# Optimization experiments

Hardware: AMD Instinct MI355X
Metric: run time of the kernel (lower is better)

The kernel has to match this reference:

```python
import jax, jax.numpy as jnp
import numpy as np

C1 = 512  # channels1 (query input dim)
C = 512   # channels (model dim)


def setup_inputs() -> dict:
    key = jax.random.key(0)
    ks = jax.random.split(key, 12)
    B, Lq, Lk = 8, 2048, 2048
    s1 = 1.0 / np.sqrt(C1)
    s = 1.0 / np.sqrt(C)
    return {
        "rep": jax.random.normal(ks[0], (B, Lq, C1), dtype=jnp.float32),
        "rep1": jax.random.normal(ks[1], (B, Lk, C), dtype=jnp.float32),
        "Wq_w": jax.random.uniform(ks[2], (C1, C), jnp.float32, -s1, s1),
        "Wq_b": jax.random.uniform(ks[3], (C,), jnp.float32, -s1, s1),
        "Wk_w": jax.random.uniform(ks[4], (C, C), jnp.float32, -s, s),
        "Wk_b": jax.random.uniform(ks[5], (C,), jnp.float32, -s, s),
        "Wv_w": jax.random.uniform(ks[6], (C, C), jnp.float32, -s, s),
        "Wv_b": jax.random.uniform(ks[7], (C,), jnp.float32, -s, s),
        "FC_w": jax.random.uniform(ks[8], (C, C), jnp.float32, -s, s),
        "FC_b": jax.random.uniform(ks[9], (C,), jnp.float32, -s, s),
    }


def reference(rep, rep1, Wq_w, Wq_b, Wk_w, Wk_b, Wv_w, Wv_b, FC_w, FC_b):
    # Linear + ReLU projections (single head)
    q = jax.nn.relu(jnp.einsum('blc,cd->bld', rep, Wq_w) + Wq_b)    # [B,Lq,C]
    k = jax.nn.relu(jnp.einsum('blc,cd->bld', rep1, Wk_w) + Wk_b)   # [B,Lk,C]
    v = jax.nn.relu(jnp.einsum('blc,cd->bld', rep1, Wv_w) + Wv_b)   # [B,Lk,C]
    scores = jnp.einsum('bqd,bkd->bqk', q, k) / jnp.sqrt(jnp.float32(C))
    attn = jax.nn.softmax(scores, axis=-1)                           # [B,Lq,Lk]
    out = jnp.einsum('bqk,bkd->bqd', attn, v)                        # [B,Lq,C]
    out = jax.nn.relu(jnp.einsum('bld,de->ble', out, FC_w) + FC_b)
    return out
```

## Files before the change

### kernel.cpp

```cpp
#include <hip/hip_runtime.h>


typedef __attribute__((ext_vector_type(8))) short short8;
typedef __attribute__((ext_vector_type(4))) float f32x4;

#define SEQ 2048
#define CH 512
#define NB 8
#define MTOT (NB * SEQ)

#define GLDS16(gp, lp)                                                                  \
  __builtin_amdgcn_global_load_lds((const __attribute__((address_space(1))) void*)(gp), \
                                   (__attribute__((address_space(3))) void*)(lp), 16, 0, 0)

__device__ __forceinline__ unsigned short f2bf(float f) {
  unsigned u = __float_as_uint(f);
  u += 0x7fffu + ((u >> 16) & 1u);
  return (unsigned short)(u >> 16);
}

__device__ __forceinline__ unsigned pack2bf(float lo, float hi) {
  return __builtin_amdgcn_perm(__float_as_uint(hi), __float_as_uint(lo), 0x07060302u);
}

#define CFENCE asm volatile("" ::: "memory")
#define SB0 __builtin_amdgcn_sched_barrier(0)
#define BAR8                          \
  do {                                \
    CFENCE;                           \
    __builtin_amdgcn_s_barrier();     \
    SB0;                              \
  } while (0)
#define VMC(n)                                              \
  do {                                                      \
    asm volatile("s_waitcnt vmcnt(" #n ")" ::: "memory");   \
    SB0;                                                    \
  } while (0)

__global__ __launch_bounds__(256) void prep2_kernel(
    const float* __restrict__ W0, const float* __restrict__ W1,
    const float* __restrict__ W2, const float* __restrict__ W3,
    unsigned short* __restrict__ Wt,
    const float* __restrict__ Wk_b, const float* __restrict__ Wv_b,
    float* __restrict__ biasKV, float* __restrict__ rowsum) {
  __shared__ __attribute__((aligned(16))) unsigned short tile[64 * 72];
  const int blk = blockIdx.x;
  const int t = threadIdx.x;
  if (blk < 256) {
    const int z = blk >> 6;
    const int bx = blk & 7, by = (blk >> 3) & 7;
    const float* W = (z == 0) ? W0 : (z == 1) ? W1 : (z == 2) ? W2 : W3;
    unsigned short* Wtz = Wt + (long)z * 512 * 512;
    const int k0 = by * 64, n0 = bx * 64;
    const int r = t >> 4, cq = (t & 15) * 4;
#pragma unroll
    for (int j = 0; j < 4; ++j) {
      int row = r + 16 * j;
      float4 v = *(const float4*)&W[(long)(k0 + row) * 512 + n0 + cq];
      tile[row * 72 + cq + 0] = f2bf(v.x);
      tile[row * 72 + cq + 1] = f2bf(v.y);
      tile[row * 72 + cq + 2] = f2bf(v.z);
      tile[row * 72 + cq + 3] = f2bf(v.w);
    }
    __syncthreads();
#pragma unroll
    for (int j = 0; j < 4; ++j) {
      int row = r + 16 * j;
      ushort4 o;
      o.x = tile[(cq + 0) * 72 + row];
      o.y = tile[(cq + 1) * 72 + row];
      o.z = tile[(cq + 2) * 72 + row];
      o.w = tile[(cq + 3) * 72 + row];
      *(ushort4*)&Wtz[(long)(n0 + row) * 512 + k0 + cq] = o;
    }
  } else if (blk == 256) {
    biasKV[t] = Wk_b[t];
    biasKV[t + 256] = Wk_b[t + 256];
    biasKV[t + 512] = Wv_b[t];
    biasKV[t + 768] = Wv_b[t + 256];
  } else {
    const int zb = blk - 257;
    f32x4 z4 = {0.f, 0.f, 0.f, 0.f};
    *(f32x4*)&rowsum[(zb * 256 + t) * 4] = z4;
  }
}

template <int LDO>
__device__ __forceinline__ void proj_body(const float* __restrict__ A,
                                          const unsigned short* __restrict__ Bt,
                                          const float* __restrict__ bias,
                                          unsigned short* __restrict__ Op,
                                          long m0, long n0, unsigned short* smem) {
  const int t = threadIdx.x;
  const int w = t >> 6, l = t & 63;
  const int wr = w >> 1, wc = w & 1;
  const int lr = l & 15, lg = l >> 4;
  const float* ga = A + (m0 + 32 * w + (l >> 3)) * CH + ((l & 7) ^ (l >> 3)) * 4;
  const unsigned short* gb =
      Bt + (n0 + 32 * w + (l >> 2)) * CH + (((l & 3) ^ ((l >> 3) & 3)) * 8);

  auto stage = [&](int c, int kt) {
    float* Ac = (float*)(smem + (long)c * 12288);
    unsigned short* Bc = smem + (long)c * 12288 + 8192;
#pragma unroll
    for (int j = 0; j < 4; ++j)
      GLDS16(ga + (long)8 * j * CH + kt * 32, Ac + (32 * w + 8 * j) * 32);
    GLDS16(gb + kt * 32, Bc + 32 * w * 32);
    GLDS16(gb + (long)16 * CH + kt * 32, Bc + (32 * w + 16) * 32);
  };

  f32x4 acc[4][4] = {};
  constexpr int NT = CH / 32;
  stage(0, 0); stage(1, 1);
  VMC(6);
  BAR8;
#pragma unroll
  for (int kt = 0; kt < NT; ++kt) {
    const int c = kt % 3;
    if (kt + 2 < NT) stage((kt + 2) % 3, kt + 2);
    const float* Ac = (const float*)(smem + (long)c * 12288);
    const unsigned short* Bc = smem + (long)c * 12288 + 8192;
    short8 af[4], bfr[4];
#pragma unroll
    for (int i = 0; i < 4; ++i) {
      const int row = 64 * wr + 16 * i + lr;
      f32x4 a0 = *(f32x4*)&Ac[row * 32 + ((2 * lg) ^ (lr & 7)) * 4];
      f32x4 a1 = *(f32x4*)&Ac[row * 32 + ((2 * lg + 1) ^ (lr & 7)) * 4];
      union { unsigned u[4]; short8 s; } pk;
      pk.u[0] = pack2bf(a0[0], a0[1]);
      pk.u[1] = pack2bf(a0[2], a0[3]);
      pk.u[2] = pack2bf(a1[0], a1[1]);
      pk.u[3] = pack2bf(a1[2], a1[3]);
      af[i] = pk.s;
      bfr[i] = *(short8*)&Bc[(64 * wc + 16 * i + lr) * 32 + (lg ^ ((lr >> 1) & 3)) * 8];
    }
#pragma unroll
    for (int mi = 0; mi < 4; ++mi)
#pragma unroll
      for (int ni = 0; ni < 4; ++ni)
        acc[mi][ni] =
            __builtin_amdgcn_mfma_f32_16x16x32_bf16(af[mi], bfr[ni], acc[mi][ni], 0, 0, 0);
    if (kt + 2 < NT) { VMC(6); } else if (kt + 1 < NT) { VMC(0); }
    BAR8;
  }
  unsigned short* patch = smem;
  float bv[4];
#pragma unroll
  for (int ni = 0; ni < 4; ++ni) bv[ni] = bias[n0 + 64 * wc + 16 * ni + lr];
#pragma unroll
  for (int mi = 0; mi < 4; ++mi)
#pragma unroll
    for (int ni = 0; ni < 4; ++ni)
#pragma unroll
      for (int r = 0; r < 4; ++r) {
        const int m = 64 * wr + 16 * mi + 4 * lg + r;
        const int n = 64 * wc + 16 * ni + lr;
        patch[m * 128 + ((n >> 3) ^ (m & 15)) * 8 + (n & 7)] =
            f2bf(fmaxf(acc[mi][ni][r] + bv[ni], 0.0f));
      }
  __syncthreads();
  const int q = t & 3;
#pragma unroll
  for (int p = 0; p < 2; ++p) {
    const int m = 64 * p + (t >> 2);
#pragma unroll
    for (int i = 0; i < 4; ++i) {
      const int cc = i * 4 + q;
      short8 x = *(short8*)&patch[m * 128 + ((cc ^ (m & 15)) * 8)];
      *(short8*)&Op[(m0 + m) * LDO + n0 + cc * 8] = x;
    }
  }
}

__global__ __launch_bounds__(256) void proj_kernel(const float* __restrict__ rep,
                                                   const float* __restrict__ rep1,
                                                   const unsigned short* __restrict__ Wt,
                                                   const float* __restrict__ Wq_b,
                                                   const float* __restrict__ biasKV,
                                                   unsigned short* __restrict__ Qb,
                                                   unsigned short* __restrict__ KVb) {
  __shared__ __attribute__((aligned(16))) unsigned short smem[36864];
  const int bid = blockIdx.x;
  const int xcd = bid & 7, j = bid >> 3;
  const int mp = j / 12, x = j % 12;
  const long m0 = (long)(xcd * 16 + mp) * 128;
  if (x < 4)
    proj_body<CH>(rep, Wt, Wq_b, Qb, m0, (long)x * 128, smem);
  else
    proj_body<1024>(rep1, Wt + 512 * 512, biasKV, KVb, m0, (long)(x - 4) * 128, smem);
}

template <int EPI, int LDA, int LDB, int LDO, int K>
__device__ __forceinline__ void gemm_body32(const unsigned short* __restrict__ A,
                                            const unsigned short* __restrict__ Bt,
                                            float* __restrict__ rowsum,
                                            void* __restrict__ outp,
                                            long m0, long n0, unsigned short* smem) {
  const int t = threadIdx.x;
  const int w = t >> 6, l = t & 63;
  const int wr = w >> 1, wc = w & 1;
  const int lr = l & 15, lg = l >> 4;
  const int srow = t >> 2;
  const int sxor = ((t & 3) ^ ((t >> 3) & 3)) * 8;
  const unsigned short* gA = A + (m0 + srow) * (long)LDA + sxor;
  const unsigned short* gB = Bt + (n0 + srow) * (long)LDB + sxor;

  auto stage = [&](int c, int kt) {
    unsigned short* Ac = smem + c * 8192;
    unsigned short* Bc = Ac + 4096;
#pragma unroll
    for (int j = 0; j < 2; ++j) {
      GLDS16(gA + (long)(64 * j) * LDA + kt * 32, Ac + (64 * j + 16 * w) * 32);
      GLDS16(gB + (long)(64 * j) * LDB + kt * 32, Bc + (64 * j + 16 * w) * 32);
    }
  };

  f32x4 acc[4][4] = {};
  constexpr int NT = K / 32;
  stage(0, 0); stage(1, 1);
  VMC(4);
  BAR8;
#pragma unroll
  for (int kt = 0; kt < NT; ++kt) {
    const int c = kt % 3;
    if (kt + 2 < NT) stage((kt + 2) % 3, kt + 2);
    const unsigned short* Ac = smem + c * 8192;
    const unsigned short* Bc = Ac + 4096;
    short8 af[4], bfr[4];
    const int kc = (lg ^ ((lr >> 1) & 3)) * 8;
#pragma unroll
    for (int i = 0; i < 4; ++i) {
      af[i]  = *(const short8*)&Ac[(64 * wr + 16 * i + lr) * 32 + kc];
      bfr[i] = *(const short8*)&Bc[(64 * wc + 16 * i + lr) * 32 + kc];
    }
#pragma unroll
    for (int mi = 0; mi < 4; ++mi)
#pragma unroll
      for (int ni = 0; ni < 4; ++ni)
        acc[mi][ni] =
            __builtin_amdgcn_mfma_f32_16x16x32_bf16(af[mi], bfr[ni], acc[mi][ni], 0, 0, 0);
    if (kt + 2 < NT) { VMC(4); } else if (kt + 1 < NT) { VMC(0); }
    BAR8;
  }

  unsigned short* patch = smem;
  float rsum[4][4] = {};
#pragma unroll
  for (int mi = 0; mi < 4; ++mi)
#pragma unroll
    for (int ni = 0; ni < 4; ++ni)
#pragma unroll
      for (int r = 0; r < 4; ++r) {
        const int m = 64 * wr + 16 * mi + 4 * lg + r;
        const int n = 64 * wc + 16 * ni + lr;
        float a = acc[mi][ni][r];
        unsigned short ob;
        if (EPI == 6) ob = f2bf(a);
        else {
          float p = exp2f(a * 0.06375872f);
          ob = f2bf(p);
          rsum[mi][r] += __uint_as_float((unsigned)ob << 16);
        }
        patch[m * 128 + ((n >> 3) ^ (m & 15)) * 8 + (n & 7)] = ob;
      }
  __syncthreads();
  unsigned short* O = (unsigned short*)outp;
  const int q = t & 3;
#pragma unroll
  for (int p = 0; p < 2; ++p) {
    const int m = 64 * p + (t >> 2);
#pragma unroll
    for (int i = 0; i < 4; ++i) {
      const int cc = i * 4 + q;
      short8 x = *(short8*)&patch[m * 128 + ((cc ^ (m & 15)) * 8)];
      *(short8*)&O[(m0 + m) * LDO + n0 + cc * 8] = x;
    }
  }
  if (EPI == 2) {
#pragma unroll
    for (int off = 1; off < 16; off <<= 1)
#pragma unroll
      for (int mi = 0; mi < 4; ++mi)
#pragma unroll
        for (int r = 0; r < 4; ++r) rsum[mi][r] += __shfl_xor(rsum[mi][r], off);
    if (lr == 0) {
#pragma unroll
      for (int mi = 0; mi < 4; ++mi)
#pragma unroll
        for (int r = 0; r < 4; ++r)
          atomicAdd(&rowsum[m0 + 64 * wr + 16 * mi + 4 * lg + r], rsum[mi][r]);
    }
  }
}

__global__ __launch_bounds__(256) void qkvf_kernel(const unsigned short* __restrict__ Qb,
                                                   const unsigned short* __restrict__ KVb,
                                                   const unsigned short* __restrict__ WtF,
                                                   float* __restrict__ rowsum,
                                                   unsigned short* __restrict__ Pbuf,
                                                   unsigned short* __restrict__ VFt) {
  __shared__ __attribute__((aligned(16))) unsigned short smem[3 * 8192];
  const int bid = blockIdx.x;
  const int bz = bid & 7, j = bid >> 3;
  const int x = j & 15, y = j >> 4;
  if (y < 16) {
    gemm_body32<2, CH, 1024, SEQ, CH>(
        Qb + (long)bz * SEQ * CH, KVb + (long)bz * SEQ * 1024,
        rowsum + (long)bz * SEQ, Pbuf + (long)bz * SEQ * SEQ,
        (long)y * 128, (long)x * 128, smem);
  } else {
    gemm_body32<6, CH, 1024, SEQ, CH>(
        WtF, KVb + 512 + (long)bz * SEQ * 1024, nullptr,
        VFt + (long)bz * CH * SEQ,
        (long)(y - 16) * 128, (long)x * 128, smem);
  }
}

#define LGKM0                                            \
  do {                                                   \
    asm volatile("s_waitcnt lgkmcnt(0)" ::: "memory");   \
    SB0;                                                 \
  } while (0)

__global__ __launch_bounds__(512, 2) void pvf_kernel(const unsigned short* __restrict__ Pbuf,
                                                     const unsigned short* __restrict__ VFt,
                                                     const float* __restrict__ FC_b,
                                                     float* __restrict__ rowsum,
                                                     float* __restrict__ out) {
  __shared__ __attribute__((aligned(16))) unsigned short smem[3][24576];
  const int s = blockIdx.x;
  const int xcd = s & 7, j = s >> 3;
  const int x = j & 3, pg = j >> 2;
  const int y = xcd, bz = pg;
  const long m0 = (long)y * 256, n0 = (long)x * 128;

  const unsigned short* A  = Pbuf + (long)bz * SEQ * SEQ;
  const unsigned short* Bt = VFt + (long)bz * CH * SEQ;
  constexpr int LDA = SEQ, LDB = SEQ;
  constexpr int NT = SEQ / 64;

  const int t = threadIdx.x;
  const int w = t >> 6, l = t & 63;
  const int wr = w >> 1, wc = w & 1;
  const int lr = l & 15, lg = l >> 4;

  const int srow = t >> 3;
  const int schk = ((t & 7) ^ ((t >> 3) & 7)) * 8;
  const unsigned short* gA = A + (m0 + srow) * (long)LDA + schk;
  const unsigned short* gB = Bt + (n0 + srow) * (long)LDB + schk;

  auto stageA = [&](int c, int kt) {
#pragma unroll
    for (int jj = 0; jj < 4; ++jj) {
      unsigned short* d = &smem[c][(64 * jj + 8 * w) * 64];
      GLDS16(gA + (long)(64 * jj) * LDA + (long)kt * 64, d);
    }
  };
  auto stageB = [&](int c, int kt) {
#pragma unroll
    for (int jj = 0; jj < 2; ++jj) {
      unsigned short* d = &smem[c][16384 + (64 * jj + 8 * w) * 64];
      GLDS16(gB + (long)(64 * jj) * LDB + (long)kt * 64, d);
    }
  };

  const int kx0 = (lg ^ (lr & 7)) * 8;
  const int kx1 = ((4 + lg) ^ (lr & 7)) * 8;
  short8 af[8], bf0[4], bf1[4];
  f32x4 acc[4][4] = {};

  auto readA = [&](int c) {
#pragma unroll
    for (int i = 0; i < 4; ++i) {
      const unsigned short* p = &smem[c][(64 * wr + 16 * i + lr) * 64];
      af[2 * i]     = *(const short8*)&p[kx0];
      af[2 * i + 1] = *(const short8*)&p[kx1];
    }
  };
  auto readB = [&](int c, int nh, short8* bf) {
#pragma unroll
    for (int i = 0; i < 2; ++i) {
      const unsigned short* p = &smem[c][16384 + (64 * wc + 16 * (2 * nh + i) + lr) * 64];
      bf[2 * i]     = *(const short8*)&p[kx0];
      bf[2 * i + 1] = *(const short8*)&p[kx1];
    }
  };
  auto quad = [&](int nh, const short8* bf) {
    __builtin_amdgcn_s_setprio(1);
#pragma unroll
    for (int mi = 0; mi < 4; ++mi)
#pragma unroll
      for (int jj = 0; jj < 2; ++jj) {
        acc[mi][2 * nh + jj] = __builtin_amdgcn_mfma_f32_16x16x32_bf16(
            af[2 * mi], bf[2 * jj], acc[mi][2 * nh + jj], 0, 0, 0);
        acc[mi][2 * nh + jj] = __builtin_amdgcn_mfma_f32_16x16x32_bf16(
            af[2 * mi + 1], bf[2 * jj + 1], acc[mi][2 * nh + jj], 0, 0, 0);
      }
    __builtin_amdgcn_s_setprio(0);
  };

  stageA(0, 0); stageB(0, 0);
  stageA(1, 1); stageB(1, 1);
  VMC(6);
  BAR8;

#pragma unroll
  for (int kt = 0; kt < NT; ++kt) {
    const int b = kt % 3, nb = (kt + 2) % 3;
    const bool st = (kt + 2) < NT;
    readA(b); readB(b, 0, bf0);
    if (st) stageA(nb, kt + 2);
    BAR8; LGKM0; quad(0, bf0); BAR8;
    readB(b, 1, bf1);
    if (st) { stageB(nb, kt + 2); VMC(6); } else { VMC(0); }
    BAR8; LGKM0; quad(1, bf1); BAR8;
  }

  __syncthreads();
  float* patchF = (float*)&smem[0][0];
  float bv[4];
#pragma unroll
  for (int ni = 0; ni < 4; ++ni) bv[ni] = FC_b[n0 + 64 * wc + 16 * ni + lr];
  float inv[4][4];
#pragma unroll
  for (int mi = 0; mi < 4; ++mi)
#pragma unroll
    for (int r = 0; r < 4; ++r)
      inv[mi][r] = 1.0f / rowsum[(long)bz * SEQ + m0 + 64 * wr + 16 * mi + 4 * lg + r];
#pragma unroll
  for (int mi = 0; mi < 4; ++mi)
#pragma unroll
    for (int ni = 0; ni < 4; ++ni)
#pragma unroll
      for (int r = 0; r < 4; ++r) {
        const int m = 64 * wr + 16 * mi + 4 * lg + r;
        const int n = 64 * wc + 16 * ni + lr;
        patchF[m * 128 + ((n >> 2) ^ (m & 31)) * 4 + (n & 3)] =
            fmaxf(acc[mi][ni][r] * inv[mi][r] + bv[ni], 0.0f);
      }
  __syncthreads();
  {
    float* O = out + (long)bz * SEQ * CH;
    const int q = t & 3, mr = t >> 2;
#pragma unroll
    for (int p2 = 0; p2 < 2; ++p2) {
      const int m = 128 * p2 + mr;
#pragma unroll
      for (int i = 0; i < 8; ++i) {
        const int cc = i * 4 + q;
        f32x4 v = *(f32x4*)&patchF[m * 128 + ((cc ^ (m & 31)) * 4)];
        *(f32x4*)&O[(m0 + m) * CH + n0 + cc * 4] = v;
      }
    }
  }
}

extern "C" void kernel_launch(void* const* d_in, const int* in_sizes, int n_in,
                              void* d_out, int out_size, void* d_ws, size_t ws_size,
                              hipStream_t stream) {
  const float* rep  = (const float*)d_in[0];
  const float* rep1 = (const float*)d_in[1];
  const float* Wq_w = (const float*)d_in[2];
  const float* Wq_b = (const float*)d_in[3];
  const float* Wk_w = (const float*)d_in[4];
  const float* Wk_b = (const float*)d_in[5];
  const float* Wv_w = (const float*)d_in[6];
  const float* Wv_b = (const float*)d_in[7];
  const float* FC_w = (const float*)d_in[8];
  const float* FC_b = (const float*)d_in[9];
  float* out = (float*)d_out;
  char* ws = (char*)d_ws;

  const size_t MB = 1024 * 1024;
  unsigned short* Qb     = (unsigned short*)(ws + 0 * MB);
  unsigned short* KVb    = (unsigned short*)(ws + 16 * MB);
  unsigned short* VFt    = (unsigned short*)(ws + 48 * MB);
  unsigned short* Wt4    = (unsigned short*)(ws + 64 * MB);
  float*          biasKV = (float*)(ws + 66 * MB);
  unsigned short* Pbuf   = (unsigned short*)(ws + 67 * MB);
  float*          rowsum = (float*)(ws + 131 * MB);
  const size_t need = 132 * MB;
  if (ws_size < need) return;

  unsigned short* WtF = Wt4 + 3 * 512 * 512;

  prep2_kernel<<<273, 256, 0, stream>>>(Wq_w, Wk_w, Wv_w, FC_w, Wt4, Wk_b, Wv_b,
                                        biasKV, rowsum);

  proj_kernel<<<1536, 256, 0, stream>>>(rep, rep1, Wt4, Wq_b, biasKV, Qb, KVb);

  qkvf_kernel<<<2560, 256, 0, stream>>>(Qb, KVb, WtF, rowsum, Pbuf, VFt);

  pvf_kernel<<<256, 512, 0, stream>>>(Pbuf, VFt, FC_b, rowsum, out);
}
```

Before: 291.8 us.

## Load A fragments directly to registers in qkvf GEMM, stage only B via LDS

The QK/VF GEMM body now reads the A operand straight from global memory into registers, double-buffered one k-step ahead, and stages only the B operand through LDS with a 3-deep ring. This halves LDS traffic and shared-memory footprint (24K to 16K shorts), which may allow higher occupancy. The launch also moves from a swizzled 1D grid to a 3D grid (x,y,z=batch), which changes block-to-XCD placement and L2 locality. In exchange, A reads now go through uncoalesced per-lane 16-byte global loads whose latency is only hidden by a single step of prefetch.

```diff
diff --git a/kernel.cpp b/kernel.cpp
--- a/kernel.cpp
+++ b/kernel.cpp
@@ -35,6 +35,11 @@
   do {                                                      \
     asm volatile("s_waitcnt vmcnt(" #n ")" ::: "memory");   \
     SB0;                                                    \
+  } while (0)
+#define LGKM0                                            \
+  do {                                                   \
+    asm volatile("s_waitcnt lgkmcnt(0)" ::: "memory");   \
+    SB0;                                                 \
   } while (0)
 
 __global__ __launch_bounds__(256) void prep2_kernel(
@@ -202,46 +207,56 @@
   const int lr = l & 15, lg = l >> 4;
   const int srow = t >> 2;
   const int sxor = ((t & 3) ^ ((t >> 3) & 3)) * 8;
-  const unsigned short* gA = A + (m0 + srow) * (long)LDA + sxor;
   const unsigned short* gB = Bt + (n0 + srow) * (long)LDB + sxor;
 
-  auto stage = [&](int c, int kt) {
-    unsigned short* Ac = smem + c * 8192;
-    unsigned short* Bc = Ac + 4096;
-#pragma unroll
-    for (int j = 0; j < 2; ++j) {
-      GLDS16(gA + (long)(64 * j) * LDA + kt * 32, Ac + (64 * j + 16 * w) * 32);
+  auto stageB = [&](int c, int kt) {
+    unsigned short* Bc = smem + c * 4096;
+#pragma unroll
+    for (int j = 0; j < 2; ++j)
       GLDS16(gB + (long)(64 * j) * LDB + kt * 32, Bc + (64 * j + 16 * w) * 32);
-    }
-  };
+  };
+
+  const unsigned short* gA = A + (m0 + 64 * wr + lr) * (long)LDA + 8 * lg;
 
   f32x4 acc[4][4] = {};
+  short8 af[2][4];
   constexpr int NT = K / 32;
-  stage(0, 0); stage(1, 1);
-  VMC(4);
+
+#pragma unroll
+  for (int i = 0; i < 4; ++i)
+    af[0][i] = *(const short8*)&gA[(long)(16 * i) * LDA];
+  SB0;
+  stageB(0, 0); stageB(1, 1);
+  VMC(2);
   BAR8;
+
 #pragma unroll
   for (int kt = 0; kt < NT; ++kt) {
-    const int c = kt % 3;
-    if (kt + 2 < NT) stage((kt + 2) % 3, kt + 2);
-    const unsigned short* Ac = smem + c * 8192;
-    const unsigned short* Bc = Ac + 4096;
-    short8 af[4], bfr[4];
+    const int cur = kt & 1, nxt = cur ^ 1;
+    if (kt + 1 < NT) {
+#pragma unroll
+      for (int i = 0; i < 4; ++i)
+        af[nxt][i] = *(const short8*)&gA[(long)(16 * i) * LDA + (kt + 1) * 32];
+    }
+    SB0;
+    if (kt + 2 < NT) stageB((kt + 2) % 3, kt + 2);
+    SB0;
+    const unsigned short* Bc = smem + (kt % 3) * 4096;
     const int kc = (lg ^ ((lr >> 1) & 3)) * 8;
-#pragma unroll
-    for (int i = 0; i < 4; ++i) {
-      af[i]  = *(const short8*)&Ac[(64 * wr + 16 * i + lr) * 32 + kc];
+    short8 bfr[4];
+#pragma unroll
+    for (int i = 0; i < 4; ++i)
       bfr[i] = *(const short8*)&Bc[(64 * wc + 16 * i + lr) * 32 + kc];
-    }
 #pragma unroll
     for (int mi = 0; mi < 4; ++mi)
 #pragma unroll
       for (int ni = 0; ni < 4; ++ni)
-        acc[mi][ni] =
-            __builtin_amdgcn_mfma_f32_16x16x32_bf16(af[mi], bfr[ni], acc[mi][ni], 0, 0, 0);
-    if (kt + 2 < NT) { VMC(4); } else if (kt + 1 < NT) { VMC(0); }
-    BAR8;
-  }
+        acc[mi][ni] = __builtin_amdgcn_mfma_f32_16x16x32_bf16(af[cur][mi], bfr[ni],
+                                                              acc[mi][ni], 0, 0, 0);
+    if (kt + 2 < NT) { VMC(2); BAR8; }
+    else if (kt + 1 < NT) { VMC(0); BAR8; }
+  }
+  BAR8;
 
   unsigned short* patch = smem;
   float rsum[4][4] = {};
@@ -299,28 +314,20 @@
                                                    float* __restrict__ rowsum,
                                                    unsigned short* __restrict__ Pbuf,
                                                    unsigned short* __restrict__ VFt) {
-  __shared__ __attribute__((aligned(16))) unsigned short smem[3 * 8192];
-  const int bid = blockIdx.x;
-  const int bz = bid & 7, j = bid >> 3;
-  const int x = j & 15, y = j >> 4;
-  if (y < 16) {
+  __shared__ __attribute__((aligned(16))) unsigned short smem[16384];
+  const int bz = blockIdx.z;
+  if (blockIdx.y < 16) {
     gemm_body32<2, CH, 1024, SEQ, CH>(
         Qb + (long)bz * SEQ * CH, KVb + (long)bz * SEQ * 1024,
         rowsum + (long)bz * SEQ, Pbuf + (long)bz * SEQ * SEQ,
-        (long)y * 128, (long)x * 128, smem);
+        (long)blockIdx.y * 128, (long)blockIdx.x * 128, smem);
   } else {
     gemm_body32<6, CH, 1024, SEQ, CH>(
         WtF, KVb + 512 + (long)bz * SEQ * 1024, nullptr,
         VFt + (long)bz * CH * SEQ,
-        (long)(y - 16) * 128, (long)x * 128, smem);
-  }
-}
-
-#define LGKM0                                            \
-  do {                                                   \
-    asm volatile("s_waitcnt lgkmcnt(0)" ::: "memory");   \
-    SB0;                                                 \
-  } while (0)
+        (long)(blockIdx.y - 16) * 128, (long)blockIdx.x * 128, smem);
+  }
+}
 
 __global__ __launch_bounds__(512, 2) void pvf_kernel(const unsigned short* __restrict__ Pbuf,
                                                      const unsigned short* __restrict__ VFt,
@@ -489,7 +496,7 @@
 
   proj_kernel<<<1536, 256, 0, stream>>>(rep, rep1, Wt4, Wq_b, biasKV, Qb, KVb);
 
-  qkvf_kernel<<<2560, 256, 0, stream>>>(Qb, KVb, WtF, rowsum, Pbuf, VFt);
+  qkvf_kernel<<<dim3(16, 20, 8), 256, 0, stream>>>(Qb, KVb, WtF, rowsum, Pbuf, VFt);
 
   pvf_kernel<<<256, 512, 0, stream>>>(Pbuf, VFt, FC_b, rowsum, out);
 }
```

Result: slower. 327.4 us (+12.2%).
